# Optimization experiments

Hardware: AMD Instinct MI355X
Metric: run time of the kernel (lower is better)

The kernel has to match this reference:

```python
import jax, jax.numpy as jnp
import numpy as np

N_HEAD = 16
WINDOW = 256
GLOBAL = 32


def _sparse_mask(T):
    # local window of +/- WINDOW//2 plus global rows/cols for first GLOBAL tokens
    i = jnp.arange(T)
    local = jnp.abs(i[:, None] - i[None, :]) <= (WINDOW // 2)
    glob = (i[:, None] < GLOBAL) | (i[None, :] < GLOBAL)
    return local | glob  # [T, T] bool


def setup_inputs() -> dict:
    key = jax.random.key(0)
    k1, k2, k3 = jax.random.split(key, 3)
    B, T, C = 1, 4096, 1024
    scale = 0.02
    return {
        "x": jax.random.normal(k1, (B, T, C), dtype=jnp.float32),
        "W_attn": jax.random.normal(k2, (C, 3 * C), dtype=jnp.float32) * scale,
        "b_attn": jnp.zeros((3 * C,), dtype=jnp.float32),
        "W_proj": jax.random.normal(k3, (C, C), dtype=jnp.float32) * scale,
        "b_proj": jnp.zeros((C,), dtype=jnp.float32),
    }


def reference(x, W_attn, b_attn, W_proj, b_proj):
    B, T, C = x.shape
    H = N_HEAD
    D = C // H

    qkv = x @ W_attn + b_attn  # [B, T, 3C]
    q, k, v = jnp.split(qkv, 3, axis=-1)
    # [B, H, T, D]
    q = q.reshape(B, T, H, D).transpose(0, 2, 1, 3)
    k = k.reshape(B, T, H, D).transpose(0, 2, 1, 3)
    v = v.reshape(B, T, H, D).transpose(0, 2, 1, 3)

    mask = _sparse_mask(T)  # [T, T]
    att = jnp.einsum("bhqd,bhkd->bhqk", q, k) * (1.0 / np.sqrt(D))
    neg = jnp.finfo(att.dtype).min
    att = jnp.where(mask, att, neg)
    att = jax.nn.softmax(att, axis=-1)
    y = jnp.einsum("bhqk,bhkd->bhqd", att, v)  # [B, H, T, D]
    y = y.transpose(0, 2, 1, 3).reshape(B, T, C)
    return y @ W_proj + b_proj
```

## Files before the change

kernel.cpp:

```cpp
#include <hip/hip_runtime.h>
#include <hip/hip_bf16.h>
#include <math.h>

#define T_SEQ 4096
#define C_DIM 1024
#define H_HEADS 16
#define D_HEAD 64
#define QKVW 3072
#define WIN_HALF 128
#define GLOBAL_TOK 32

typedef __attribute__((ext_vector_type(8))) short bf16x8;
typedef __attribute__((ext_vector_type(4))) float f32x4;

__device__ __forceinline__ float bf2f(unsigned short u) {
    union { unsigned int i; float f; } c; c.i = ((unsigned int)u) << 16; return c.f;
}
__device__ __forceinline__ unsigned short f2bf(float f) {
    union { float f; unsigned int i; } c; c.f = f;
    return (unsigned short)((c.i + 0x7fffu + ((c.i >> 16) & 1u)) >> 16);
}

__device__ __forceinline__ void gll16(const unsigned short* g, unsigned short* l) {
    __builtin_amdgcn_global_load_lds(
        (const __attribute__((address_space(1))) void*)g,
        (__attribute__((address_space(3))) void*)l, 16, 0, 0);
}

__device__ __forceinline__ int swz(int row, int chunk) {
    return row * 64 + ((chunk ^ (row & 7)) * 8);
}

__global__ __launch_bounds__(256) void prep_kernel(
    const float* __restrict__ x, const float* __restrict__ Wa,
    const float* __restrict__ Wp,
    unsigned short* __restrict__ xb, unsigned short* __restrict__ Wabt,
    unsigned short* __restrict__ Wpbt)
{
    __shared__ unsigned short tile[32][36];
    const int bid = blockIdx.x;
    const int t = threadIdx.x;
    if (bid < 4096) {
        const int idx = bid * 256 + t;
        float4 v = ((const float4*)x)[idx];
        ushort4 o;
        o.x = f2bf(v.x); o.y = f2bf(v.y); o.z = f2bf(v.z); o.w = f2bf(v.w);
        ((ushort4*)xb)[idx] = o;
        return;
    }
    const float* src; unsigned short* dst; int R, Ncols, bx, by;
    if (bid < 4096 + 3072) {
        const int b = bid - 4096;
        src = Wa; dst = Wabt; R = C_DIM; Ncols = QKVW;
        bx = b % (QKVW / 32); by = b / (QKVW / 32);
    } else {
        const int b = bid - 7168;
        src = Wp; dst = Wpbt; R = C_DIM; Ncols = C_DIM;
        bx = b % (C_DIM / 32); by = b / (C_DIM / 32);
    }
    const int r0 = by * 32, c0 = bx * 32;
    const int rr = t >> 3, cq = (t & 7) * 4;
    float4 v = *(const float4*)(src + (size_t)(r0 + rr) * Ncols + c0 + cq);
    tile[rr][cq + 0] = f2bf(v.x); tile[rr][cq + 1] = f2bf(v.y);
    tile[rr][cq + 2] = f2bf(v.z); tile[rr][cq + 3] = f2bf(v.w);
    __syncthreads();
    const int cc = t >> 3, rq = (t & 7) * 4;
    ushort4 o;
    o.x = tile[rq + 0][cc]; o.y = tile[rq + 1][cc];
    o.z = tile[rq + 2][cc]; o.w = tile[rq + 3][cc];
    *(ushort4*)(dst + (size_t)(c0 + cc) * R + r0 + rq) = o;
}

template<int OUT_BF16, int WRITE_VT>
__global__ __launch_bounds__(256) void gemm_nt_kernel(
    const unsigned short* __restrict__ A,
    const unsigned short* __restrict__ Bt,
    const float* __restrict__ bias,
    void* __restrict__ Cv, unsigned short* __restrict__ vTp,
    int M, int N, int K)
{
    __shared__ unsigned short As[128 * 32];
    __shared__ unsigned short Bs[128 * 32];
    const int tid = threadIdx.x;
    const int w = tid >> 6, lane = tid & 63;
    const int quad = lane >> 4, r16 = lane & 15;
    const int nbx = gridDim.x;
    const int nwg = nbx * gridDim.y;
    int lb = blockIdx.y * nbx + blockIdx.x;
    lb = (lb & 7) * (nwg >> 3) + (lb >> 3);
    const int m0 = (lb / nbx) * 128, n0 = (lb % nbx) * 128;
    const int wm = (w & 1) * 64, wn = (w >> 1) * 64;

    f32x4 acc[4][4];
    #pragma unroll
    for (int i = 0; i < 4; ++i)
        #pragma unroll
        for (int j = 0; j < 4; ++j) acc[i][j] = (f32x4){0.f, 0.f, 0.f, 0.f};

    const unsigned short* Ab = A + (size_t)m0 * K;
    const unsigned short* Bb = Bt + (size_t)n0 * K;

    for (int k0 = 0; k0 < K; k0 += 32) {
        __syncthreads();
        #pragma unroll
        for (int i = 0; i < 2; ++i) {
            const int chunk = w * 128 + i * 64 + lane;
            const int row = chunk >> 2, kc = (chunk & 3) * 8;
            gll16(Ab + (size_t)row * K + k0 + kc, &As[(w * 2 + i) * 512]);
            gll16(Bb + (size_t)row * K + k0 + kc, &Bs[(w * 2 + i) * 512]);
        }
        asm volatile("s_waitcnt vmcnt(0)" ::: "memory");
        __builtin_amdgcn_sched_barrier(0);
        __syncthreads();

        bf16x8 af[4], bf_[4];
        #pragma unroll
        for (int t = 0; t < 4; ++t) {
            af[t]  = *(const bf16x8*)&As[(wm + t * 16 + r16) * 32 + quad * 8];
            bf_[t] = *(const bf16x8*)&Bs[(wn + t * 16 + r16) * 32 + quad * 8];
        }
        #pragma unroll
        for (int mt = 0; mt < 4; ++mt)
            #pragma unroll
            for (int nt = 0; nt < 4; ++nt)
                acc[mt][nt] = __builtin_amdgcn_mfma_f32_16x16x32_bf16(
                    af[mt], bf_[nt], acc[mt][nt], 0, 0, 0);
    }

    if (WRITE_VT && n0 >= 2 * C_DIM) {
        #pragma unroll
        for (int nt = 0; nt < 4; ++nt) {
            const int col = n0 + wn + nt * 16 + r16;
            const float bv = bias[col];
            const int vcol = col - 2 * C_DIM;
            #pragma unroll
            for (int mt = 0; mt < 4; ++mt) {
                ushort4 o;
                o.x = f2bf(acc[mt][nt][0] + bv);
                o.y = f2bf(acc[mt][nt][1] + bv);
                o.z = f2bf(acc[mt][nt][2] + bv);
                o.w = f2bf(acc[mt][nt][3] + bv);
                *(ushort4*)&vTp[(size_t)vcol * T_SEQ + m0 + wm + mt * 16 + quad * 4] = o;
            }
        }
    } else {
        #pragma unroll
        for (int nt = 0; nt < 4; ++nt) {
            const int col = n0 + wn + nt * 16 + r16;
            const float bv = bias[col];
            #pragma unroll
            for (int mt = 0; mt < 4; ++mt)
                #pragma unroll
                for (int reg = 0; reg < 4; ++reg) {
                    const int row = m0 + wm + mt * 16 + quad * 4 + reg;
                    if (OUT_BF16)
                        ((unsigned short*)Cv)[(size_t)row * N + col] = f2bf(acc[mt][nt][reg] + bv);
                    else
                        ((float*)Cv)[(size_t)row * N + col] = acc[mt][nt][reg] + bv;
                }
        }
    }
}

#define PT_STRIDE 72
#define NSLOT 8
#define PROW 72

struct KVbuf { bf16x8 kl[4], kh[4], vl[4], vh[4]; };
struct StReg { bf16x8 a, b, c, d; };

#define LOAD_KV(C0, B)                                                         \
  {                                                                            \
    const unsigned short* kr_ = kb + (size_t)((C0) + n) * QKVW + quad * 8;     \
    _Pragma("unroll")                                                          \
    for (int g = 0; g < 4; ++g) {                                              \
      B.kl[g] = *(const bf16x8*)(kr_ + (size_t)(g * 16) * QKVW);               \
      B.kh[g] = *(const bf16x8*)(kr_ + (size_t)(g * 16) * QKVW + 32);          \
    }                                                                          \
    const unsigned short* vr_ = vb + (size_t)n * T_SEQ + (C0) + quad * 8;      \
    _Pragma("unroll")                                                          \
    for (int d = 0; d < 4; ++d) {                                              \
      B.vl[d] = *(const bf16x8*)(vr_ + (size_t)(d * 16) * T_SEQ);              \
      B.vh[d] = *(const bf16x8*)(vr_ + (size_t)(d * 16) * T_SEQ + 32);         \
    }                                                                          \
  }

#define SOFTMAX_P_UPDATE(StV)                                                  \
    mm = fmaxf(mm, __shfl_xor(mm, 16));                                        \
    mm = fmaxf(mm, __shfl_xor(mm, 32));                                        \
    const float mn = fmaxf(m_run, mm);                                         \
    const float mnf = (mn == -INFINITY) ? 0.f : mn;                            \
    const float al = __expf(m_run - mnf);                                      \
    float rs = 0.f;                                                            \
    _Pragma("unroll")                                                          \
    for (int g = 0; g < 4; ++g) {                                              \
      const float e0 = __expf(StV[g][0] - mnf);                                \
      const float e1 = __expf(StV[g][1] - mnf);                                \
      const float e2 = __expf(StV[g][2] - mnf);                                \
      const float e3 = __expf(StV[g][3] - mnf);                                \
      rs += (e0 + e1) + (e2 + e3);                                             \
      const unsigned int p01 = f2bf(e0) | ((unsigned int)f2bf(e1) << 16);      \
      const unsigned int p23 = f2bf(e2) | ((unsigned int)f2bf(e3) << 16);      \
      *(unsigned int*)&myPt[n * PT_STRIDE + g * 16 + quad * 4] = p01;          \
      *(unsigned int*)&myPt[n * PT_STRIDE + g * 16 + quad * 4 + 2] = p23;      \
    }                                                                          \
    rs += __shfl_xor(rs, 16);                                                  \
    rs += __shfl_xor(rs, 32);                                                  \
    l_run = l_run * al + rs;                                                   \
    m_run = mn;                                                                \
    _Pragma("unroll")                                                          \
    for (int d = 0; d < 4; ++d)                                                \
      _Pragma("unroll")                                                        \
      for (int r = 0; r < 4; ++r) O[d][r] *= al;

#define PROC_TILE(ITV, CUR, NXT)                                               \
  {                                                                            \
    const int it_ = (ITV);                                                     \
    const int c0 = split * 512 + it_ * 64;                                     \
    f32x4 St[4];                                                               \
    __builtin_amdgcn_s_setprio(1);                                             \
    _Pragma("unroll")                                                          \
    for (int g = 0; g < 4; ++g) {                                              \
      St[g] = __builtin_amdgcn_mfma_f32_16x16x32_bf16(CUR.kl[g], q0, Zf, 0, 0, 0); \
      St[g] = __builtin_amdgcn_mfma_f32_16x16x32_bf16(CUR.kh[g], q1, St[g], 0, 0, 0); \
    }                                                                          \
    __builtin_amdgcn_s_setprio(0);                                             \
    if (it_ + 1 < n_tiles) {                                                   \
      LOAD_KV(c0 + 64, NXT);                                                   \
    }                                                                          \
    float mm = -INFINITY;                                                      \
    _Pragma("unroll")                                                          \
    for (int g = 0; g < 4; ++g)                                                \
      _Pragma("unroll")                                                        \
      for (int r = 0; r < 4; ++r) {                                            \
        const float v = St[g][r] * 0.125f;                                     \
        St[g][r] = v; mm = fmaxf(mm, v);                                       \
      }                                                                        \
    SOFTMAX_P_UPDATE(St)                                                       \
    asm volatile("s_waitcnt lgkmcnt(0)" ::: "memory");                         \
    __builtin_amdgcn_sched_barrier(0);                                         \
    __builtin_amdgcn_s_setprio(1);                                             \
    _Pragma("unroll")                                                          \
    for (int kg = 0; kg < 2; ++kg) {                                           \
      bf16x8 pf_ = *(const bf16x8*)&myPt[n * PT_STRIDE + kg * 32 + quad * 8];  \
      _Pragma("unroll")                                                        \
      for (int d = 0; d < 4; ++d)                                              \
        O[d] = __builtin_amdgcn_mfma_f32_16x16x32_bf16(                        \
            kg ? CUR.vh[d] : CUR.vl[d], pf_, O[d], 0, 0, 0);                   \
    }                                                                          \
    __builtin_amdgcn_s_setprio(0);                                             \
  }

#define STAGE_LOAD(C0, R)                                                      \
  { const int c0s_ = (C0);                                                     \
    R.a = *(const bf16x8*)(kb + (size_t)(c0s_ + srow) * QKVW + scol * 8);      \
    R.b = *(const bf16x8*)(kb + (size_t)(c0s_ + srow + 32) * QKVW + scol * 8); \
    R.c = *(const bf16x8*)(vb + (size_t)srow * T_SEQ + c0s_ + scol * 8);       \
    R.d = *(const bf16x8*)(vb + (size_t)(srow + 32) * T_SEQ + c0s_ + scol * 8); }

#define STAGE_WRITE(BUF, R)                                                    \
  { *(bf16x8*)&Ks[BUF][kdst0] = R.a;                                           \
    *(bf16x8*)&Ks[BUF][kdst1] = R.b;                                           \
    *(bf16x8*)&Vs[BUF][kdst0] = R.c;                                           \
    *(bf16x8*)&Vs[BUF][kdst1] = R.d; }

#define WTILE(ITV, BUF, RW, RL)                                                \
  {                                                                            \
    const int it_ = (ITV);                                                     \
    const int c0 = (it_ == 0) ? 0 : (blo + (it_ - 1) * 64);                    \
    if (activeW) {                                                             \
      bf16x8 kl[4], kh[4];                                                     \
      _Pragma("unroll")                                                        \
      for (int g = 0; g < 4; ++g) {                                            \
        kl[g] = *(const bf16x8*)&Ks[BUF][swz(n + g * 16, quad)];               \
        kh[g] = *(const bf16x8*)&Ks[BUF][swz(n + g * 16, quad + 4)];           \
      }                                                                        \
      f32x4 St[4];                                                             \
      __builtin_amdgcn_s_setprio(1);                                           \
      _Pragma("unroll")                                                        \
      for (int g = 0; g < 4; ++g) {                                            \
        St[g] = __builtin_amdgcn_mfma_f32_16x16x32_bf16(kl[g], q0, Zf, 0, 0, 0); \
        St[g] = __builtin_amdgcn_mfma_f32_16x16x32_bf16(kh[g], q1, St[g], 0, 0, 0); \
      }                                                                        \
      __builtin_amdgcn_s_setprio(0);                                           \
      float mm = -INFINITY;                                                    \
      if (it_ != 0 && c0 >= rowbase - 113 && c0 <= rowbase + 65) {             \
        _Pragma("unroll")                                                      \
        for (int g = 0; g < 4; ++g)                                            \
          _Pragma("unroll")                                                    \
          for (int r = 0; r < 4; ++r) {                                        \
            const float v = St[g][r] * 0.125f;                                 \
            St[g][r] = v; mm = fmaxf(mm, v);                                   \
          }                                                                    \
      } else if (it_ == 0 && rowbase >= 192) {                                 \
        _Pragma("unroll")                                                      \
        for (int g = 0; g < 2; ++g)                                            \
          _Pragma("unroll")                                                    \
          for (int r = 0; r < 4; ++r) {                                        \
            const float v = St[g][r] * 0.125f;                                 \
            St[g][r] = v; mm = fmaxf(mm, v);                                   \
          }                                                                    \
        _Pragma("unroll")                                                      \
        for (int g = 2; g < 4; ++g)                                            \
          _Pragma("unroll")                                                    \
          for (int r = 0; r < 4; ++r) St[g][r] = -INFINITY;                    \
      } else {                                                                 \
        _Pragma("unroll")                                                      \
        for (int g = 0; g < 4; ++g)                                            \
          _Pragma("unroll")                                                    \
          for (int r = 0; r < 4; ++r) {                                        \
            float v = St[g][r] * 0.125f;                                       \
            const int col = c0 + g * 16 + quad * 4 + r;                        \
            int dd = row - col; dd = dd < 0 ? -dd : dd;                        \
            if (!(col < GLOBAL_TOK || dd <= WIN_HALF)) v = -INFINITY;          \
            St[g][r] = v; mm = fmaxf(mm, v);                                   \
          }                                                                    \
      }                                                                        \
      SOFTMAX_P_UPDATE(St)                                                     \
      bf16x8 vl[4], vh[4];                                                     \
      _Pragma("unroll")                                                        \
      for (int d = 0; d < 4; ++d) {                                            \
        vl[d] = *(const bf16x8*)&Vs[BUF][swz(n + d * 16, quad)];               \
        vh[d] = *(const bf16x8*)&Vs[BUF][swz(n + d * 16, quad + 4)];           \
      }                                                                        \
      asm volatile("s_waitcnt lgkmcnt(0)" ::: "memory");                       \
      __builtin_amdgcn_sched_barrier(0);                                       \
      __builtin_amdgcn_s_setprio(1);                                           \
      _Pragma("unroll")                                                        \
      for (int kg = 0; kg < 2; ++kg) {                                         \
        bf16x8 pf_ = *(const bf16x8*)&myPt[n * PT_STRIDE + kg * 32 + quad * 8];\
        _Pragma("unroll")                                                      \
        for (int d = 0; d < 4; ++d)                                            \
          O[d] = __builtin_amdgcn_mfma_f32_16x16x32_bf16(                      \
              kg ? vh[d] : vl[d], pf_, O[d], 0, 0, 0);                         \
      }                                                                        \
      __builtin_amdgcn_s_setprio(0);                                           \
    }                                                                          \
    if (it_ + 1 < NT) {                                                        \
      asm volatile("s_waitcnt vmcnt(0)" ::: "memory");                         \
      __builtin_amdgcn_sched_barrier(0);                                       \
      STAGE_WRITE((BUF) ^ 1, RW);                                              \
      if (it_ + 2 < NT) { STAGE_LOAD(blo + (it_ + 1) * 64, RL); }              \
      __syncthreads();                                                         \
    }                                                                          \
  }

__global__ __launch_bounds__(256, 3) void sparse_attn_mfma(
    const unsigned short* __restrict__ qkv,
    const unsigned short* __restrict__ vT,
    unsigned short* __restrict__ y,
    float* __restrict__ part)
{
    __shared__ unsigned short Ks[2][64 * 64];
    __shared__ unsigned short Vs[2][64 * 64];
    __shared__ unsigned short Pt[4][16 * PT_STRIDE];
    const int tid = threadIdx.x;
    const int w = tid >> 6, lane = tid & 63;
    const int quad = lane >> 4, n = lane & 15;
    const int bid = blockIdx.x;
    const f32x4 Zf = (f32x4){0.f, 0.f, 0.f, 0.f};

    if (bid < 1024) {
        const int h = bid & 15;
        const int B = bid >> 4;
        const int base = B * 64;
        const int rowbase = base + w * 16;
        const bool activeW = !(B == 0 && w < 2);
        int blo = base - 128; if (blo < 64) blo = 64;
        int bhi = base + 192; if (bhi > T_SEQ) bhi = T_SEQ;
        const int NT = 1 + (bhi - blo) / 64;

        const unsigned short* kb = qkv + C_DIM + h * 64;
        const unsigned short* vb = vT + (size_t)h * 64 * T_SEQ;
        unsigned short* myPt = Pt[w];

        const int srow = tid >> 3, scol = tid & 7;
        const int kdst0 = swz(srow, scol);
        const int kdst1 = kdst0 + 32 * 64;

        const unsigned short* qp = qkv + (size_t)(rowbase + n) * QKVW + h * 64 + quad * 8;
        bf16x8 q0 = *(const bf16x8*)qp;
        bf16x8 q1 = *(const bf16x8*)(qp + 32);

        f32x4 O[4];
        #pragma unroll
        for (int i = 0; i < 4; ++i) O[i] = (f32x4){0.f, 0.f, 0.f, 0.f};
        float m_run = -INFINITY, l_run = 0.f;
        const int row = rowbase + n;

        StReg r0, r1;
        STAGE_LOAD(0, r0);
        asm volatile("s_waitcnt vmcnt(0)" ::: "memory");
        __builtin_amdgcn_sched_barrier(0);
        STAGE_WRITE(0, r0);
        STAGE_LOAD(blo, r1);
        __syncthreads();

        int it = 0;
        for (;;) {
            WTILE(it, 0, r1, r0);
            if (++it >= NT) break;
            WTILE(it, 1, r0, r1);
            if (++it >= NT) break;
        }

        if (activeW) {
            const float invL = 1.f / l_run;
            #pragma unroll
            for (int dblk = 0; dblk < 4; ++dblk)
                #pragma unroll
                for (int r = 0; r < 4; ++r)
                    y[(size_t)row * C_DIM + h * 64 + dblk * 16 + quad * 4 + r] =
                        f2bf(O[dblk][r] * invL);
        }
    } else {
        const int idx = bid - 1024;
        const int h = idx & 15;
        const int u = (idx >> 4) * 4 + w;
        const int rt = u >> 3, split = u & 7;
        const int rowbase = rt * 16;
        const int n_tiles = 8;

        const unsigned short* qp = qkv + (size_t)(rowbase + n) * QKVW + h * 64 + quad * 8;
        bf16x8 q0 = *(const bf16x8*)qp;
        bf16x8 q1 = *(const bf16x8*)(qp + 32);

        const unsigned short* kb = qkv + C_DIM + h * 64;
        const unsigned short* vb = vT + (size_t)h * 64 * T_SEQ;
        unsigned short* myPt = Pt[w];

        f32x4 O[4];
        #pragma unroll
        for (int i = 0; i < 4; ++i) O[i] = (f32x4){0.f, 0.f, 0.f, 0.f};
        float m_run = -INFINITY, l_run = 0.f;

        KVbuf b0, b1;
        LOAD_KV(split * 512, b0);
        int it = 0;
        for (;;) {
            PROC_TILE(it, b0, b1);
            if (++it >= n_tiles) break;
            PROC_TILE(it, b1, b0);
            if (++it >= n_tiles) break;
        }

        float* pb = part + ((size_t)(h * 2 + rt) * NSLOT + split) * 16 * PROW;
        #pragma unroll
        for (int dblk = 0; dblk < 4; ++dblk)
            #pragma unroll
            for (int r = 0; r < 4; ++r)
                pb[n * PROW + dblk * 16 + quad * 4 + r] = O[dblk][r];
        if (quad == 0) {
            pb[n * PROW + 64] = m_run;
            pb[n * PROW + 65] = l_run;
        }
    }
}

__global__ __launch_bounds__(64) void attn_combine(
    const float* __restrict__ part, unsigned short* __restrict__ y)
{
    const int d = threadIdx.x;
    const int h = blockIdx.x >> 1, rt = blockIdx.x & 1;
    const float* base = part + (size_t)(h * 2 + rt) * NSLOT * 16 * PROW;
    for (int row = 0; row < 16; ++row) {
        float M = -INFINITY;
        for (int sl = 0; sl < NSLOT; ++sl)
            M = fmaxf(M, base[(size_t)sl * 16 * PROW + row * PROW + 64]);
        float L = 0.f, Od = 0.f;
        for (int sl = 0; sl < NSLOT; ++sl) {
            const float* p = base + (size_t)sl * 16 * PROW + row * PROW;
            const float s = __expf(p[64] - M);
            L += p[65] * s;
            Od += p[d] * s;
        }
        y[(size_t)(rt * 16 + row) * C_DIM + h * 64 + d] = f2bf(Od / L);
    }
}

extern "C" void kernel_launch(void* const* d_in, const int* in_sizes, int n_in,
                              void* d_out, int out_size, void* d_ws, size_t ws_size,
                              hipStream_t stream) {
    const float* x  = (const float*)d_in[0];
    const float* Wa = (const float*)d_in[1];
    const float* ba = (const float*)d_in[2];
    const float* Wp = (const float*)d_in[3];
    const float* bp = (const float*)d_in[4];
    float* out = (float*)d_out;

    unsigned short* xb   = (unsigned short*)d_ws;
    unsigned short* Wabt = xb   + (size_t)T_SEQ * C_DIM;
    unsigned short* Wpbt = Wabt + (size_t)C_DIM * QKVW;
    unsigned short* qkv  = Wpbt + (size_t)C_DIM * C_DIM;
    unsigned short* yat  = qkv  + (size_t)T_SEQ * QKVW;
    unsigned short* vT   = yat  + (size_t)T_SEQ * C_DIM;
    float* part = (float*)(vT + (size_t)C_DIM * T_SEQ);

    prep_kernel<<<4096 + 3072 + 1024, 256, 0, stream>>>(
        x, Wa, Wp, xb, Wabt, Wpbt);

    gemm_nt_kernel<1, 1><<<dim3(QKVW / 128, T_SEQ / 128), 256, 0, stream>>>(
        xb, Wabt, ba, qkv, vT, T_SEQ, QKVW, C_DIM);

    const int nBlocks = 1024 + 64;
    sparse_attn_mfma<<<nBlocks, 256, 0, stream>>>(qkv, vT, yat, part);
    attn_combine<<<H_HEADS * 2, 64, 0, stream>>>(part, yat);

    gemm_nt_kernel<0, 0><<<dim3(C_DIM / 128, T_SEQ / 128), 256, 0, stream>>>(
        yat, Wpbt, bp, out, nullptr, T_SEQ, C_DIM, C_DIM);
}
```

Before: 206.7 us.

## Double-buffer GEMM LDS tiles and drop workgroup index swizzle

Splits the GEMM's LDS staging into two buffers so the global-to-LDS load for the next K slice is issued before the MFMAs on the current slice, aiming to hide global load latency behind compute. It also removes the block-index remapping that grouped workgroups for cache locality and uses plain blockIdx tiling instead. The extra buffer doubles LDS use per block, which may lower occupancy. Losing the swizzle may hurt L2 reuse. Correctness relies on K being a multiple of 64.

```diff
diff --git a/kernel.cpp b/kernel.cpp
--- a/kernel.cpp
+++ b/kernel.cpp
@@ -71,6 +71,37 @@
     *(ushort4*)(dst + (size_t)(c0 + cc) * R + r0 + rq) = o;
 }
 
+#define GSTAGE(BUF, KO)                                                        \
+  _Pragma("unroll")                                                            \
+  for (int i = 0; i < 2; ++i) {                                                \
+    const int chunk = w * 128 + i * 64 + lane;                                 \
+    const int row = chunk >> 2, kc = (chunk & 3) * 8;                          \
+    gll16(Ab + (size_t)row * K + (KO) + kc, &As[BUF][(w * 2 + i) * 512]);      \
+    gll16(Bb + (size_t)row * K + (KO) + kc, &Bs[BUF][(w * 2 + i) * 512]);      \
+  }
+
+#define GSTEP(K0, CURB, NXTB)                                                  \
+  {                                                                            \
+    if ((K0) + 32 < K) { GSTAGE(NXTB, (K0) + 32); }                            \
+    bf16x8 af[4], bf_[4];                                                      \
+    _Pragma("unroll")                                                          \
+    for (int t = 0; t < 4; ++t) {                                              \
+      af[t]  = *(const bf16x8*)&As[CURB][(wm + t * 16 + r16) * 32 + quad * 8]; \
+      bf_[t] = *(const bf16x8*)&Bs[CURB][(wn + t * 16 + r16) * 32 + quad * 8]; \
+    }                                                                          \
+    _Pragma("unroll")                                                          \
+    for (int mt = 0; mt < 4; ++mt)                                             \
+      _Pragma("unroll")                                                        \
+      for (int nt = 0; nt < 4; ++nt)                                           \
+        acc[mt][nt] = __builtin_amdgcn_mfma_f32_16x16x32_bf16(                 \
+            af[mt], bf_[nt], acc[mt][nt], 0, 0, 0);                            \
+    if ((K0) + 32 < K) {                                                       \
+      asm volatile("s_waitcnt vmcnt(0)" ::: "memory");                         \
+      __builtin_amdgcn_sched_barrier(0);                                       \
+      __syncthreads();                                                         \
+    }                                                                          \
+  }
+
 template<int OUT_BF16, int WRITE_VT>
 __global__ __launch_bounds__(256) void gemm_nt_kernel(
     const unsigned short* __restrict__ A,
@@ -79,16 +110,12 @@
     void* __restrict__ Cv, unsigned short* __restrict__ vTp,
     int M, int N, int K)
 {
-    __shared__ unsigned short As[128 * 32];
-    __shared__ unsigned short Bs[128 * 32];
+    __shared__ unsigned short As[2][128 * 32];
+    __shared__ unsigned short Bs[2][128 * 32];
     const int tid = threadIdx.x;
     const int w = tid >> 6, lane = tid & 63;
     const int quad = lane >> 4, r16 = lane & 15;
-    const int nbx = gridDim.x;
-    const int nwg = nbx * gridDim.y;
-    int lb = blockIdx.y * nbx + blockIdx.x;
-    lb = (lb & 7) * (nwg >> 3) + (lb >> 3);
-    const int m0 = (lb / nbx) * 128, n0 = (lb % nbx) * 128;
+    const int m0 = blockIdx.y * 128, n0 = blockIdx.x * 128;
     const int wm = (w & 1) * 64, wn = (w >> 1) * 64;
 
     f32x4 acc[4][4];
@@ -100,31 +127,14 @@
     const unsigned short* Ab = A + (size_t)m0 * K;
     const unsigned short* Bb = Bt + (size_t)n0 * K;
 
-    for (int k0 = 0; k0 < K; k0 += 32) {
-        __syncthreads();
-        #pragma unroll
-        for (int i = 0; i < 2; ++i) {
-            const int chunk = w * 128 + i * 64 + lane;
-            const int row = chunk >> 2, kc = (chunk & 3) * 8;
-            gll16(Ab + (size_t)row * K + k0 + kc, &As[(w * 2 + i) * 512]);
-            gll16(Bb + (size_t)row * K + k0 + kc, &Bs[(w * 2 + i) * 512]);
-        }
-        asm volatile("s_waitcnt vmcnt(0)" ::: "memory");
-        __builtin_amdgcn_sched_barrier(0);
-        __syncthreads();
-
-        bf16x8 af[4], bf_[4];
-        #pragma unroll
-        for (int t = 0; t < 4; ++t) {
-            af[t]  = *(const bf16x8*)&As[(wm + t * 16 + r16) * 32 + quad * 8];
-            bf_[t] = *(const bf16x8*)&Bs[(wn + t * 16 + r16) * 32 + quad * 8];
-        }
-        #pragma unroll
-        for (int mt = 0; mt < 4; ++mt)
-            #pragma unroll
-            for (int nt = 0; nt < 4; ++nt)
-                acc[mt][nt] = __builtin_amdgcn_mfma_f32_16x16x32_bf16(
-                    af[mt], bf_[nt], acc[mt][nt], 0, 0, 0);
+    GSTAGE(0, 0);
+    asm volatile("s_waitcnt vmcnt(0)" ::: "memory");
+    __builtin_amdgcn_sched_barrier(0);
+    __syncthreads();
+
+    for (int k0 = 0; k0 < K; k0 += 64) {
+        GSTEP(k0, 0, 1);
+        GSTEP(k0 + 32, 1, 0);
     }
 
     if (WRITE_VT && n0 >= 2 * C_DIM) {
```

Measured after the change: 215.1 us. 1.04x slower.
